# Performance work log

Hardware: AMD Instinct MI355X
Metric: run time of the kernel (lower is better)

The kernel has to match this reference:

```python
import jax, jax.numpy as jnp
import numpy as np

N, E, F_IN, H, C, G, NC = 50000, 800000, 128, 4, 64, 512, 10
NEG_SLOPE = 0.2


def setup_inputs() -> dict:
    key = jax.random.key(0)
    ks = jax.random.split(key, 16)
    s = lambda fan: 1.0 / np.sqrt(fan)
    inp = {
        'x': jax.random.normal(ks[0], (N, F_IN), jnp.float32),
        'edge_index': jax.random.randint(ks[1], (2, E), 0, N, jnp.int64),
        'batch': jnp.sort(jax.random.randint(ks[2], (N,), 0, G, jnp.int64)),
        # conv1: F_IN -> H*C, concat
        'W1': jax.random.normal(ks[3], (F_IN, H * C), jnp.float32) * s(F_IN),
        'a_src1': jax.random.normal(ks[4], (H, C), jnp.float32) * s(C),
        'a_dst1': jax.random.normal(ks[5], (H, C), jnp.float32) * s(C),
        'b1': jnp.zeros((H * C,), jnp.float32),
        # conv2: H*C -> H*C, concat
        'W2': jax.random.normal(ks[6], (H * C, H * C), jnp.float32) * s(H * C),
        'a_src2': jax.random.normal(ks[7], (H, C), jnp.float32) * s(C),
        'a_dst2': jax.random.normal(ks[8], (H, C), jnp.float32) * s(C),
        'b2': jnp.zeros((H * C,), jnp.float32),
        # conv3: H*C -> C, concat=False (mean over heads)
        'W3': jax.random.normal(ks[9], (H * C, H * C), jnp.float32) * s(H * C),
        'a_src3': jax.random.normal(ks[10], (H, C), jnp.float32) * s(C),
        'a_dst3': jax.random.normal(ks[11], (H, C), jnp.float32) * s(C),
        'b3': jnp.zeros((C,), jnp.float32),
        # final linear: C -> NC
        'Wl': jax.random.normal(ks[12], (C, NC), jnp.float32) * s(C),
        'bl': jnp.zeros((NC,), jnp.float32),
    }
    return inp


def _gat_conv(x, src, dst, W, a_src, a_dst, b, concat):
    n = x.shape[0]
    h = (x @ W).reshape(n, H, C)                       # [N,H,C]
    al_src = jnp.sum(h * a_src, axis=-1)               # [N,H]
    al_dst = jnp.sum(h * a_dst, axis=-1)               # [N,H]
    e = al_src[src] + al_dst[dst]                      # [E',H] per-edge logits
    e = jax.nn.leaky_relu(e, NEG_SLOPE)
    # segment softmax over incoming edges of each dst node
    m = jax.ops.segment_max(e, dst, num_segments=n)
    ex = jnp.exp(e - m[dst])
    z = jax.ops.segment_sum(ex, dst, num_segments=n)
    alpha = ex / (z[dst] + 1e-16)                      # [E',H]
    msg = h[src] * alpha[:, :, None]                   # [E',H,C]
    out = jax.ops.segment_sum(msg, dst, num_segments=n)  # [N,H,C]
    out = out.reshape(n, H * C) if concat else out.mean(axis=1)
    return out + b


def reference(x, edge_index, batch, W1, a_src1, a_dst1, b1, W2, a_src2, a_dst2, b2,
              W3, a_src3, a_dst3, b3, Wl, bl):
    n = x.shape[0]
    loops = jnp.arange(n, dtype=edge_index.dtype)
    src = jnp.concatenate([edge_index[0], loops])      # add self-loops (PyG default)
    dst = jnp.concatenate([edge_index[1], loops])
    h = jax.nn.relu(_gat_conv(x, src, dst, W1, a_src1, a_dst1, b1, True))
    h = jax.nn.relu(_gat_conv(h, src, dst, W2, a_src2, a_dst2, b2, True))
    h = jax.nn.relu(_gat_conv(h, src, dst, W3, a_src3, a_dst3, b3, False))
    # global mean pool over graphs
    sums = jax.ops.segment_sum(h, batch, num_segments=G)          # [G,C]
    cnts = jax.ops.segment_sum(jnp.ones((n,), h.dtype), batch, num_segments=G)
    pooled = sums / jnp.maximum(cnts, 1.0)[:, None]
    # dropout is identity in eval mode
    return pooled @ Wl + bl                                       # [G,NC]
```

## Files before the change

### kernel.cpp

```cpp
#include <hip/hip_runtime.h>

#define N_NODES 50000
#define E_EDGES 800000
#define E_TOT   (E_EDGES + N_NODES)
#define F_INDIM 128
#define NHEAD   4
#define CDIM    64
#define HC      256
#define NGRAPH  512
#define NCLS    10
#define NEG_SLOPE 0.2f
#define AGG_BLOCKS 2048
#define XCHUNKS (N_NODES * F_INDIM / 8)

typedef __attribute__((ext_vector_type(8))) _Float16 f16x8;
typedef __attribute__((ext_vector_type(8))) unsigned short ushort8;
typedef __attribute__((ext_vector_type(4))) float f32x4;

__device__ inline float leakyf(float x) { return x > 0.f ? x : NEG_SLOPE * x; }
__device__ inline unsigned short f2h(float x) {
  _Float16 h = (_Float16)x;
  return __builtin_bit_cast(unsigned short, h);
}
__device__ inline float h2f(unsigned short u) {
  return (float)__builtin_bit_cast(_Float16, u);
}

__global__ __launch_bounds__(256) void k_init_deg(int* __restrict__ deg) {
  int i = blockIdx.x * 256 + threadIdx.x;
  if (i < N_NODES) deg[i] = 1;
}

__global__ __launch_bounds__(256) void k_hist(const int* __restrict__ ei, int* __restrict__ deg) {
  int e = blockIdx.x * 256 + threadIdx.x;
  if (e < E_EDGES) atomicAdd(&deg[ei[E_EDGES + e]], 1);
}

__global__ __launch_bounds__(256) void k_scan1(const int* __restrict__ deg, int* __restrict__ incl,
                                               int* __restrict__ blksum) {
  __shared__ int s[256];
  int tid = threadIdx.x;
  int i = blockIdx.x * 256 + tid;
  int v = (i < N_NODES) ? deg[i] : 0;
  s[tid] = v;
  __syncthreads();
  for (int d = 1; d < 256; d <<= 1) {
    int t = (tid >= d) ? s[tid - d] : 0;
    __syncthreads();
    s[tid] += t;
    __syncthreads();
  }
  if (i < N_NODES) incl[i] = s[tid];
  if (tid == 255) blksum[blockIdx.x] = s[255];
}

__global__ __launch_bounds__(256) void k_scan2(int* __restrict__ blksum, int nblk) {
  __shared__ int s[256];
  int tid = threadIdx.x;
  int v = (tid < nblk) ? blksum[tid] : 0;
  s[tid] = v;
  __syncthreads();
  for (int d = 1; d < 256; d <<= 1) {
    int t = (tid >= d) ? s[tid - d] : 0;
    __syncthreads();
    s[tid] += t;
    __syncthreads();
  }
  if (tid < nblk) blksum[tid] = s[tid] - v;
}

__global__ __launch_bounds__(256) void k_scan3(const int* __restrict__ deg, int* __restrict__ off,
                                               const int* __restrict__ blksum, int* __restrict__ cursor) {
  int i = blockIdx.x * 256 + threadIdx.x;
  if (i < N_NODES) {
    int excl = off[i] - deg[i] + blksum[blockIdx.x];
    off[i] = excl;
    cursor[i] = excl;
  }
  if (i == 0) off[N_NODES] = E_TOT;
}

__global__ __launch_bounds__(256) void k_fill(const int* __restrict__ ei, int* __restrict__ cursor,
                                              int* __restrict__ csr_src) {
  int idx = blockIdx.x * 256 + threadIdx.x;
  if (idx >= E_TOT) return;
  int s, d;
  if (idx < E_EDGES) { s = ei[idx]; d = ei[E_EDGES + idx]; }
  else               { s = idx - E_EDGES; d = s; }
  int pos = atomicAdd(&cursor[d], 1);
  csr_src[pos] = s;
}

__global__ __launch_bounds__(256) void k_cvt_all(const float* __restrict__ x,
                                                 const float* __restrict__ W1,
                                                 const float* __restrict__ W2,
                                                 const float* __restrict__ W3,
                                                 unsigned short* __restrict__ xh,
                                                 unsigned short* __restrict__ Wt1,
                                                 unsigned short* __restrict__ Wt2,
                                                 unsigned short* __restrict__ Wt3) {
  int i = blockIdx.x * 256 + threadIdx.x;
  if (i < XCHUNKS) {
    float4 v0 = *(const float4*)&x[(size_t)i * 8];
    float4 v1 = *(const float4*)&x[(size_t)i * 8 + 4];
    ushort8 o;
    o[0] = f2h(v0.x); o[1] = f2h(v0.y); o[2] = f2h(v0.z); o[3] = f2h(v0.w);
    o[4] = f2h(v1.x); o[5] = f2h(v1.y); o[6] = f2h(v1.z); o[7] = f2h(v1.w);
    *(ushort8*)&xh[(size_t)i * 8] = o;
    return;
  }
  int j = i - XCHUNKS;
  if (j < F_INDIM * HC) {
    int k = j >> 8, n = j & 255;
    Wt1[n * F_INDIM + k] = f2h(W1[j]);
    return;
  }
  j -= F_INDIM * HC;
  if (j < HC * HC) {
    int k = j >> 8, n = j & 255;
    Wt2[n * HC + k] = f2h(W2[j]);
    return;
  }
  j -= HC * HC;
  if (j < HC * HC) {
    int k = j >> 8, n = j & 255;
    Wt3[n * HC + k] = f2h(W3[j]);
  }
}

template<int K>
__global__ __launch_bounds__(256) void k_gemm_f16(const unsigned short* __restrict__ A,
                                                  const unsigned short* __restrict__ Bt,
                                                  unsigned short* __restrict__ C,
                                                  const float* __restrict__ a_src,
                                                  const float* __restrict__ a_dst,
                                                  float* __restrict__ al_s,
                                                  float* __restrict__ al_d) {
  __shared__ unsigned short As[128 * 64];
  __shared__ unsigned short Bs[128 * 64];
  int tid = threadIdx.x;
  int w = tid >> 6, l = tid & 63;
  int wm = w >> 1, wn = w & 1;
  int m0 = blockIdx.x * 128, n0 = blockIdx.y * 128;
  f32x4 acc[4][4] = {};

  int sr = w * 32 + (l >> 3);
  int g8 = l & 7;
  int slot = g8 ^ (sr & 7);
  int fl = l & 15;

  for (int k0 = 0; k0 < K; k0 += 64) {
    uint4 va[4], vb[4];
#pragma unroll
    for (int j = 0; j < 4; ++j) {
      int ar = m0 + sr + j * 8;
      va[j] = (ar < N_NODES) ? *(const uint4*)&A[(size_t)ar * K + k0 + g8 * 8]
                             : make_uint4(0u, 0u, 0u, 0u);
      vb[j] = *(const uint4*)&Bt[(size_t)(n0 + sr + j * 8) * K + k0 + g8 * 8];
    }
    __syncthreads();
#pragma unroll
    for (int j = 0; j < 4; ++j) {
      *(uint4*)&As[(sr + j * 8) * 64 + slot * 8] = va[j];
      *(uint4*)&Bs[(sr + j * 8) * 64 + slot * 8] = vb[j];
    }
    __syncthreads();
#pragma unroll
    for (int kk = 0; kk < 2; ++kk) {
      int sl = ((kk * 4 + (l >> 4)) ^ (l & 7)) * 8;
      f16x8 af[4], bfr[4];
#pragma unroll
      for (int f = 0; f < 4; ++f) {
        af[f]  = *(const f16x8*)&As[(wm * 64 + f * 16 + fl) * 64 + sl];
        bfr[f] = *(const f16x8*)&Bs[(wn * 64 + f * 16 + fl) * 64 + sl];
      }
#pragma unroll
      for (int f = 0; f < 4; ++f)
#pragma unroll
        for (int g = 0; g < 4; ++g)
          acc[f][g] = __builtin_amdgcn_mfma_f32_16x16x32_f16(af[f], bfr[g], acc[f][g], 0, 0, 0);
    }
  }
  int cr = (l >> 4) * 4;
#pragma unroll
  for (int f = 0; f < 4; ++f) {
    int mrow = m0 + wm * 64 + f * 16 + cr;
#pragma unroll
    for (int r = 0; r < 4; ++r) {
      if (mrow + r < N_NODES) {
#pragma unroll
        for (int g = 0; g < 4; ++g)
          C[(size_t)(mrow + r) * HC + n0 + wn * 64 + g * 16 + fl] = f2h(acc[f][g][r]);
      }
    }
  }
  int head = blockIdx.y * 2 + wn;
  float as_r[4], ad_r[4];
#pragma unroll
  for (int g = 0; g < 4; ++g) {
    as_r[g] = a_src[head * 64 + g * 16 + fl];
    ad_r[g] = a_dst[head * 64 + g * 16 + fl];
  }
#pragma unroll
  for (int f = 0; f < 4; ++f) {
#pragma unroll
    for (int r = 0; r < 4; ++r) {
      float ps = 0.f, pd = 0.f;
#pragma unroll
      for (int g = 0; g < 4; ++g) {
        ps = fmaf(as_r[g], acc[f][g][r], ps);
        pd = fmaf(ad_r[g], acc[f][g][r], pd);
      }
#pragma unroll
      for (int o = 1; o < 16; o <<= 1) { ps += __shfl_xor(ps, o); pd += __shfl_xor(pd, o); }
      if (fl == 0) {
        int row = m0 + wm * 64 + f * 16 + cr + r;
        if (row < N_NODES) {
          al_s[row * 4 + head] = ps;
          al_d[row * 4 + head] = pd;
        }
      }
    }
  }
}

template<bool CONCAT>
__global__ __launch_bounds__(256) void k_aggregate(
    const unsigned short* __restrict__ h, const int* __restrict__ off, const int* __restrict__ csr_src,
    const float* __restrict__ al_s, const float* __restrict__ al_d,
    const float* __restrict__ bias, unsigned short* __restrict__ out_h, float* __restrict__ out_f) {
  __shared__ float s_p[4][64][4];
  __shared__ int   s_src[4][64];
  int tid = threadIdx.x;
  int wv = tid >> 6;
  int lane = tid & 63;
  int half_id = lane >> 5;
  int c8 = lane & 31;
  int cg8 = c8 << 3;
  int head = c8 >> 3;

  const int NW = AGG_BLOCKS * 4;
  for (int d = blockIdx.x * 4 + wv; d < N_NODES; d += NW) {
    int lo  = off[d];
    int deg = off[d + 1] - lo;

    float4 adv = *(const float4*)&al_d[(size_t)d * 4];

    float z0 = 0.f, z1 = 0.f, z2 = 0.f, z3 = 0.f;
    for (int e = lane; e < deg; e += 64) {
      int s = csr_src[lo + e];
      float4 asv = *(const float4*)&al_s[(size_t)s * 4];
      float p0 = __expf(leakyf(asv.x + adv.x));
      float p1 = __expf(leakyf(asv.y + adv.y));
      float p2 = __expf(leakyf(asv.z + adv.z));
      float p3 = __expf(leakyf(asv.w + adv.w));
      if (e < 64) {
        s_p[wv][e][0] = p0; s_p[wv][e][1] = p1;
        s_p[wv][e][2] = p2; s_p[wv][e][3] = p3;
        s_src[wv][e] = s;
      }
      z0 += p0; z1 += p1; z2 += p2; z3 += p3;
    }
#pragma unroll
    for (int o = 1; o < 64; o <<= 1) {
      z0 += __shfl_xor(z0, o); z1 += __shfl_xor(z1, o);
      z2 += __shfl_xor(z2, o); z3 += __shfl_xor(z3, o);
    }
    float zih = 1.f / ((head == 0 ? z0 : (head == 1 ? z1 : (head == 2 ? z2 : z3))) + 1e-16f);

    int dcap = min(deg, 64);
    float acc[8] = {};
    int e = half_id;
    for (; e + 14 < dcap; e += 16) {
      int sv[8]; float pv[8]; ushort8 hv[8];
#pragma unroll
      for (int q = 0; q < 8; ++q) {
        int ee = e + q * 2;
        sv[q] = s_src[wv][ee];
        pv[q] = s_p[wv][ee][head];
      }
#pragma unroll
      for (int q = 0; q < 8; ++q) hv[q] = *(const ushort8*)&h[(size_t)sv[q] * HC + cg8];
#pragma unroll
      for (int q = 0; q < 8; ++q)
#pragma unroll
        for (int i = 0; i < 8; ++i) acc[i] = fmaf(pv[q], h2f(hv[q][i]), acc[i]);
    }
    for (; e < dcap; e += 2) {
      int s = s_src[wv][e];
      float p = s_p[wv][e][head];
      ushort8 hv = *(const ushort8*)&h[(size_t)s * HC + cg8];
#pragma unroll
      for (int i = 0; i < 8; ++i) acc[i] = fmaf(p, h2f(hv[i]), acc[i]);
    }
    if (deg > 64) {
      for (int e2 = 64 + half_id; e2 < deg; e2 += 2) {
        int s = csr_src[lo + e2];
        float4 asv = *(const float4*)&al_s[(size_t)s * 4];
        float q0 = __expf(leakyf(asv.x + adv.x));
        float q1 = __expf(leakyf(asv.y + adv.y));
        float q2 = __expf(leakyf(asv.z + adv.z));
        float q3 = __expf(leakyf(asv.w + adv.w));
        float p = head == 0 ? q0 : (head == 1 ? q1 : (head == 2 ? q2 : q3));
        ushort8 hv = *(const ushort8*)&h[(size_t)s * HC + cg8];
#pragma unroll
        for (int i = 0; i < 8; ++i) acc[i] = fmaf(p, h2f(hv[i]), acc[i]);
      }
    }

#pragma unroll
    for (int i = 0; i < 8; ++i) {
      acc[i] *= zih;
      acc[i] += __shfl_xor(acc[i], 32);
    }

    if (CONCAT) {
      if (lane < 32) {
        float4 b0 = *(const float4*)&bias[cg8];
        float4 b1v = *(const float4*)&bias[cg8 + 4];
        ushort8 o;
        o[0] = f2h(fmaxf(acc[0] + b0.x, 0.f));
        o[1] = f2h(fmaxf(acc[1] + b0.y, 0.f));
        o[2] = f2h(fmaxf(acc[2] + b0.z, 0.f));
        o[3] = f2h(fmaxf(acc[3] + b0.w, 0.f));
        o[4] = f2h(fmaxf(acc[4] + b1v.x, 0.f));
        o[5] = f2h(fmaxf(acc[5] + b1v.y, 0.f));
        o[6] = f2h(fmaxf(acc[6] + b1v.z, 0.f));
        o[7] = f2h(fmaxf(acc[7] + b1v.w, 0.f));
        *(ushort8*)&out_h[(size_t)d * HC + cg8] = o;
      }
    } else {
#pragma unroll
      for (int i = 0; i < 8; ++i) {
        acc[i] += __shfl_xor(acc[i], 8);
        acc[i] += __shfl_xor(acc[i], 16);
      }
      if (lane < 8) {
        int c0 = lane << 3;
        float4 bb0 = *(const float4*)&bias[c0];
        float4 bb1 = *(const float4*)&bias[c0 + 4];
        float4 v0, v1;
        v0.x = fmaxf(acc[0] * 0.25f + bb0.x, 0.f);
        v0.y = fmaxf(acc[1] * 0.25f + bb0.y, 0.f);
        v0.z = fmaxf(acc[2] * 0.25f + bb0.z, 0.f);
        v0.w = fmaxf(acc[3] * 0.25f + bb0.w, 0.f);
        v1.x = fmaxf(acc[4] * 0.25f + bb1.x, 0.f);
        v1.y = fmaxf(acc[5] * 0.25f + bb1.y, 0.f);
        v1.z = fmaxf(acc[6] * 0.25f + bb1.z, 0.f);
        v1.w = fmaxf(acc[7] * 0.25f + bb1.w, 0.f);
        *(float4*)&out_f[(size_t)d * CDIM + c0] = v0;
        *(float4*)&out_f[(size_t)d * CDIM + c0 + 4] = v1;
      }
    }
  }
}

__device__ inline int lower_bound_i(const int* __restrict__ a, int n, int key) {
  int lo = 0, hi = n;
  while (lo < hi) { int mid = (lo + hi) >> 1; if (a[mid] < key) lo = mid + 1; else hi = mid; }
  return lo;
}

__global__ __launch_bounds__(256) void k_pool(const float* __restrict__ x, const int* __restrict__ batch,
                                              const float* __restrict__ Wl, const float* __restrict__ bl,
                                              float* __restrict__ out) {
  int g = blockIdx.x, tid = threadIdx.x;
  int lo = lower_bound_i(batch, N_NODES, g);
  int hi = lower_bound_i(batch, N_NODES, g + 1);
  int c = tid & 63, sl = tid >> 6;
  float acc = 0.f;
  for (int n = lo + sl; n < hi; n += 4)
    acc += x[(size_t)n * CDIM + c];
  __shared__ float s[256];
  __shared__ float pooled[64];
  s[tid] = acc;
  __syncthreads();
  if (tid < 64) {
    float cnt = fmaxf((float)(hi - lo), 1.f);
    pooled[tid] = (s[tid] + s[tid + 64] + s[tid + 128] + s[tid + 192]) / cnt;
  }
  __syncthreads();
  if (tid < NCLS) {
    float o = bl[tid];
    for (int cc = 0; cc < CDIM; ++cc)
      o = fmaf(pooled[cc], Wl[cc * NCLS + tid], o);
    out[g * NCLS + tid] = o;
  }
}

extern "C" void kernel_launch(void* const* d_in, const int* in_sizes, int n_in,
                              void* d_out, int out_size, void* d_ws, size_t ws_size,
                              hipStream_t stream) {
  const float* x     = (const float*)d_in[0];
  const int*   ei    = (const int*)d_in[1];
  const int*   batch = (const int*)d_in[2];
  const float* W1  = (const float*)d_in[3];
  const float* as1 = (const float*)d_in[4];
  const float* ad1 = (const float*)d_in[5];
  const float* b1  = (const float*)d_in[6];
  const float* W2  = (const float*)d_in[7];
  const float* as2 = (const float*)d_in[8];
  const float* ad2 = (const float*)d_in[9];
  const float* b2  = (const float*)d_in[10];
  const float* W3  = (const float*)d_in[11];
  const float* as3 = (const float*)d_in[12];
  const float* ad3 = (const float*)d_in[13];
  const float* b3  = (const float*)d_in[14];
  const float* Wl  = (const float*)d_in[15];
  const float* bl  = (const float*)d_in[16];
  float* out = (float*)d_out;

  char* ws = (char*)d_ws;
  size_t o = 0;
  auto alloc = [&](size_t bytes) -> void* {
    void* p = ws + o;
    o += (bytes + 255) & ~(size_t)255;
    return p;
  };
  unsigned short* hbuf  = (unsigned short*)alloc((size_t)N_NODES * HC * 2);
  unsigned short* abuf  = (unsigned short*)alloc((size_t)N_NODES * HC * 2);
  float*          bufC  = (float*)alloc((size_t)N_NODES * CDIM * 4);
  unsigned short* x_h   = (unsigned short*)alloc((size_t)N_NODES * F_INDIM * 2);
  unsigned short* Wt1   = (unsigned short*)alloc((size_t)HC * F_INDIM * 2);
  unsigned short* Wt2   = (unsigned short*)alloc((size_t)HC * HC * 2);
  unsigned short* Wt3   = (unsigned short*)alloc((size_t)HC * HC * 2);
  float* al_s  = (float*)alloc((size_t)N_NODES * 4 * 4);
  float* al_d  = (float*)alloc((size_t)N_NODES * 4 * 4);
  int*   deg   = (int*)alloc((size_t)N_NODES * 4);
  int*   off   = (int*)alloc((size_t)(N_NODES + 1) * 4);
  int*   cursor= (int*)alloc((size_t)N_NODES * 4);
  int*   blksum= (int*)alloc(1024);
  int*   csr   = (int*)alloc((size_t)E_TOT * 4);

  int nblk = (N_NODES + 255) / 256;
  k_init_deg<<<nblk, 256, 0, stream>>>(deg);
  k_hist<<<(E_EDGES + 255) / 256, 256, 0, stream>>>(ei, deg);
  k_scan1<<<nblk, 256, 0, stream>>>(deg, off, blksum);
  k_scan2<<<1, 256, 0, stream>>>(blksum, nblk);
  k_scan3<<<nblk, 256, 0, stream>>>(deg, off, blksum, cursor);
  k_fill<<<(E_TOT + 255) / 256, 256, 0, stream>>>(ei, cursor, csr);

  int cvt_total = XCHUNKS + F_INDIM * HC + 2 * HC * HC;
  k_cvt_all<<<(cvt_total + 255) / 256, 256, 0, stream>>>(x, W1, W2, W3, x_h, Wt1, Wt2, Wt3);

  dim3 ggrid((N_NODES + 127) / 128, HC / 128);
  k_gemm_f16<F_INDIM><<<ggrid, 256, 0, stream>>>(x_h, Wt1, hbuf, as1, ad1, al_s, al_d);
  k_aggregate<true><<<AGG_BLOCKS, 256, 0, stream>>>(hbuf, off, csr, al_s, al_d, b1, abuf, nullptr);
  k_gemm_f16<HC><<<ggrid, 256, 0, stream>>>(abuf, Wt2, hbuf, as2, ad2, al_s, al_d);
  k_aggregate<true><<<AGG_BLOCKS, 256, 0, stream>>>(hbuf, off, csr, al_s, al_d, b2, abuf, nullptr);
  k_gemm_f16<HC><<<ggrid, 256, 0, stream>>>(abuf, Wt3, hbuf, as3, ad3, al_s, al_d);
  k_aggregate<false><<<AGG_BLOCKS, 256, 0, stream>>>(hbuf, off, csr, al_s, al_d, b3, nullptr, bufC);
  k_pool<<<NGRAPH, 256, 0, stream>>>(bufC, batch, Wl, bl, out);
}
```

Measured before the change: 442.0 us.

## Store node features in per-32-channel slices and aggregate slice-by-slice

GEMM outputs and aggregation buffers now use a sliced layout ([8 slices][N][32] in fp16), and attention logits are stored head-major. The aggregation kernel gives each block one 32-channel slice, so gathered rows are 64 bytes and the slice's working set is smaller and more cache-friendly. Softmax normalization is folded into a single pass without a separate max or staging in shared memory. The head-mean, bias and ReLU of layer 3 move into the pool kernel. In exchange, each edge's index and exponent are recomputed once per slice (eight times), and gathers become small 4-byte accesses per lane.

```diff
diff --git a/kernel.cpp b/kernel.cpp
--- a/kernel.cpp
+++ b/kernel.cpp
@@ -128,7 +128,7 @@
   }
 }
 
-template<int K>
+template<int K, bool ASL>
 __global__ __launch_bounds__(256) void k_gemm_f16(const unsigned short* __restrict__ A,
                                                   const unsigned short* __restrict__ Bt,
                                                   unsigned short* __restrict__ C,
@@ -151,12 +151,18 @@
 
   for (int k0 = 0; k0 < K; k0 += 64) {
     uint4 va[4], vb[4];
+    int k = k0 + g8 * 8;
 #pragma unroll
     for (int j = 0; j < 4; ++j) {
       int ar = m0 + sr + j * 8;
-      va[j] = (ar < N_NODES) ? *(const uint4*)&A[(size_t)ar * K + k0 + g8 * 8]
-                             : make_uint4(0u, 0u, 0u, 0u);
-      vb[j] = *(const uint4*)&Bt[(size_t)(n0 + sr + j * 8) * K + k0 + g8 * 8];
+      if (ar >= N_NODES) {
+        va[j] = make_uint4(0u, 0u, 0u, 0u);
+      } else if (ASL) {
+        va[j] = *(const uint4*)&A[(size_t)(k >> 5) * N_NODES * 32 + (size_t)ar * 32 + (k & 31)];
+      } else {
+        va[j] = *(const uint4*)&A[(size_t)ar * K + k];
+      }
+      vb[j] = *(const uint4*)&Bt[(size_t)(n0 + sr + j * 8) * K + k];
     }
     __syncthreads();
 #pragma unroll
@@ -182,6 +188,7 @@
     }
   }
   int cr = (l >> 4) * 4;
+  int cb5 = (n0 + wn * 64) >> 5;
 #pragma unroll
   for (int f = 0; f < 4; ++f) {
     int mrow = m0 + wm * 64 + f * 16 + cr;
@@ -190,7 +197,8 @@
       if (mrow + r < N_NODES) {
 #pragma unroll
         for (int g = 0; g < 4; ++g)
-          C[(size_t)(mrow + r) * HC + n0 + wn * 64 + g * 16 + fl] = f2h(acc[f][g][r]);
+          C[(size_t)(cb5 + (g >> 1)) * N_NODES * 32 + (size_t)(mrow + r) * 32 + (g & 1) * 16 + fl]
+            = f2h(acc[f][g][r]);
       }
     }
   }
@@ -216,8 +224,8 @@
       if (fl == 0) {
         int row = m0 + wm * 64 + f * 16 + cr + r;
         if (row < N_NODES) {
-          al_s[row * 4 + head] = ps;
-          al_d[row * 4 + head] = pd;
+          al_s[head * N_NODES + row] = ps;
+          al_d[head * N_NODES + row] = pd;
         }
       }
     }
@@ -225,132 +233,75 @@
 }
 
 template<bool CONCAT>
-__global__ __launch_bounds__(256) void k_aggregate(
-    const unsigned short* __restrict__ h, const int* __restrict__ off, const int* __restrict__ csr_src,
-    const float* __restrict__ al_s, const float* __restrict__ al_d,
-    const float* __restrict__ bias, unsigned short* __restrict__ out_h, float* __restrict__ out_f) {
-  __shared__ float s_p[4][64][4];
-  __shared__ int   s_src[4][64];
+__global__ __launch_bounds__(256) void k_gather(
+    const unsigned short* __restrict__ h_sl, const int* __restrict__ off,
+    const int* __restrict__ csr_src,
+    const float* __restrict__ al_s_t, const float* __restrict__ al_d_t,
+    const float* __restrict__ bias, unsigned short* __restrict__ out_sl) {
   int tid = threadIdx.x;
-  int wv = tid >> 6;
-  int lane = tid & 63;
-  int half_id = lane >> 5;
-  int c8 = lane & 31;
-  int cg8 = c8 << 3;
-  int head = c8 >> 3;
-
-  const int NW = AGG_BLOCKS * 4;
-  for (int d = blockIdx.x * 4 + wv; d < N_NODES; d += NW) {
-    int lo  = off[d];
+  int wv = tid >> 6, lane = tid & 63;
+  int grp = lane >> 4;
+  int cl = lane & 15;
+  int slice = blockIdx.x & 7;
+  int head = slice >> 1;
+  const unsigned short* __restrict__ hs = h_sl + (size_t)slice * N_NODES * 32;
+  const float* __restrict__ als = al_s_t + (size_t)head * N_NODES;
+  const float* __restrict__ ald = al_d_t + (size_t)head * N_NODES;
+  unsigned short* __restrict__ os = out_sl + (size_t)slice * N_NODES * 32;
+  float b0 = 0.f, b1 = 0.f;
+  if (CONCAT) {
+    b0 = bias[slice * 32 + cl * 2];
+    b1 = bias[slice * 32 + cl * 2 + 1];
+  }
+  int wave_g = (blockIdx.x >> 3) * 4 + wv;
+
+  for (int d = wave_g; d < N_NODES; d += (AGG_BLOCKS / 8) * 4) {
+    int lo = off[d];
     int deg = off[d + 1] - lo;
-
-    float4 adv = *(const float4*)&al_d[(size_t)d * 4];
-
-    float z0 = 0.f, z1 = 0.f, z2 = 0.f, z3 = 0.f;
-    for (int e = lane; e < deg; e += 64) {
+    float ad = ald[d];
+    float a0 = 0.f, a1 = 0.f, z = 0.f;
+    int e = grp;
+    for (; e + 12 < deg; e += 16) {
+      int sv[4]; unsigned int hv[4]; float pv[4];
+#pragma unroll
+      for (int q = 0; q < 4; ++q) sv[q] = csr_src[lo + e + q * 4];
+#pragma unroll
+      for (int q = 0; q < 4; ++q) hv[q] = *(const unsigned int*)&hs[(size_t)sv[q] * 32 + cl * 2];
+#pragma unroll
+      for (int q = 0; q < 4; ++q) pv[q] = __expf(leakyf(als[sv[q]] + ad));
+#pragma unroll
+      for (int q = 0; q < 4; ++q) {
+        z += pv[q];
+        a0 = fmaf(pv[q], h2f((unsigned short)(hv[q] & 0xffffu)), a0);
+        a1 = fmaf(pv[q], h2f((unsigned short)(hv[q] >> 16)), a1);
+      }
+    }
+    for (; e < deg; e += 4) {
       int s = csr_src[lo + e];
-      float4 asv = *(const float4*)&al_s[(size_t)s * 4];
-      float p0 = __expf(leakyf(asv.x + adv.x));
-      float p1 = __expf(leakyf(asv.y + adv.y));
-      float p2 = __expf(leakyf(asv.z + adv.z));
-      float p3 = __expf(leakyf(asv.w + adv.w));
-      if (e < 64) {
-        s_p[wv][e][0] = p0; s_p[wv][e][1] = p1;
-        s_p[wv][e][2] = p2; s_p[wv][e][3] = p3;
-        s_src[wv][e] = s;
-      }
-      z0 += p0; z1 += p1; z2 += p2; z3 += p3;
-    }
-#pragma unroll
-    for (int o = 1; o < 64; o <<= 1) {
-      z0 += __shfl_xor(z0, o); z1 += __shfl_xor(z1, o);
-      z2 += __shfl_xor(z2, o); z3 += __shfl_xor(z3, o);
-    }
-    float zih = 1.f / ((head == 0 ? z0 : (head == 1 ? z1 : (head == 2 ? z2 : z3))) + 1e-16f);
-
-    int dcap = min(deg, 64);
-    float acc[8] = {};
-    int e = half_id;
-    for (; e + 14 < dcap; e += 16) {
-      int sv[8]; float pv[8]; ushort8 hv[8];
-#pragma unroll
-      for (int q = 0; q < 8; ++q) {
-        int ee = e + q * 2;
-        sv[q] = s_src[wv][ee];
-        pv[q] = s_p[wv][ee][head];
-      }
-#pragma unroll
-      for (int q = 0; q < 8; ++q) hv[q] = *(const ushort8*)&h[(size_t)sv[q] * HC + cg8];
-#pragma unroll
-      for (int q = 0; q < 8; ++q)
-#pragma unroll
-        for (int i = 0; i < 8; ++i) acc[i] = fmaf(pv[q], h2f(hv[q][i]), acc[i]);
-    }
-    for (; e < dcap; e += 2) {
-      int s = s_src[wv][e];
-      float p = s_p[wv][e][head];
-      ushort8 hv = *(const ushort8*)&h[(size_t)s * HC + cg8];
-#pragma unroll
-      for (int i = 0; i < 8; ++i) acc[i] = fmaf(p, h2f(hv[i]), acc[i]);
-    }
-    if (deg > 64) {
-      for (int e2 = 64 + half_id; e2 < deg; e2 += 2) {
-        int s = csr_src[lo + e2];
-        float4 asv = *(const float4*)&al_s[(size_t)s * 4];
-        float q0 = __expf(leakyf(asv.x + adv.x));
-        float q1 = __expf(leakyf(asv.y + adv.y));
-        float q2 = __expf(leakyf(asv.z + adv.z));
-        float q3 = __expf(leakyf(asv.w + adv.w));
-        float p = head == 0 ? q0 : (head == 1 ? q1 : (head == 2 ? q2 : q3));
-        ushort8 hv = *(const ushort8*)&h[(size_t)s * HC + cg8];
-#pragma unroll
-        for (int i = 0; i < 8; ++i) acc[i] = fmaf(p, h2f(hv[i]), acc[i]);
-      }
-    }
-
-#pragma unroll
-    for (int i = 0; i < 8; ++i) {
-      acc[i] *= zih;
-      acc[i] += __shfl_xor(acc[i], 32);
-    }
-
-    if (CONCAT) {
-      if (lane < 32) {
-        float4 b0 = *(const float4*)&bias[cg8];
-        float4 b1v = *(const float4*)&bias[cg8 + 4];
-        ushort8 o;
-        o[0] = f2h(fmaxf(acc[0] + b0.x, 0.f));
-        o[1] = f2h(fmaxf(acc[1] + b0.y, 0.f));
-        o[2] = f2h(fmaxf(acc[2] + b0.z, 0.f));
-        o[3] = f2h(fmaxf(acc[3] + b0.w, 0.f));
-        o[4] = f2h(fmaxf(acc[4] + b1v.x, 0.f));
-        o[5] = f2h(fmaxf(acc[5] + b1v.y, 0.f));
-        o[6] = f2h(fmaxf(acc[6] + b1v.z, 0.f));
-        o[7] = f2h(fmaxf(acc[7] + b1v.w, 0.f));
-        *(ushort8*)&out_h[(size_t)d * HC + cg8] = o;
-      }
-    } else {
-#pragma unroll
-      for (int i = 0; i < 8; ++i) {
-        acc[i] += __shfl_xor(acc[i], 8);
-        acc[i] += __shfl_xor(acc[i], 16);
-      }
-      if (lane < 8) {
-        int c0 = lane << 3;
-        float4 bb0 = *(const float4*)&bias[c0];
-        float4 bb1 = *(const float4*)&bias[c0 + 4];
-        float4 v0, v1;
-        v0.x = fmaxf(acc[0] * 0.25f + bb0.x, 0.f);
-        v0.y = fmaxf(acc[1] * 0.25f + bb0.y, 0.f);
-        v0.z = fmaxf(acc[2] * 0.25f + bb0.z, 0.f);
-        v0.w = fmaxf(acc[3] * 0.25f + bb0.w, 0.f);
-        v1.x = fmaxf(acc[4] * 0.25f + bb1.x, 0.f);
-        v1.y = fmaxf(acc[5] * 0.25f + bb1.y, 0.f);
-        v1.z = fmaxf(acc[6] * 0.25f + bb1.z, 0.f);
-        v1.w = fmaxf(acc[7] * 0.25f + bb1.w, 0.f);
-        *(float4*)&out_f[(size_t)d * CDIM + c0] = v0;
-        *(float4*)&out_f[(size_t)d * CDIM + c0 + 4] = v1;
-      }
+      unsigned int hv = *(const unsigned int*)&hs[(size_t)s * 32 + cl * 2];
+      float p = __expf(leakyf(als[s] + ad));
+      z += p;
+      a0 = fmaf(p, h2f((unsigned short)(hv & 0xffffu)), a0);
+      a1 = fmaf(p, h2f((unsigned short)(hv >> 16)), a1);
+    }
+#pragma unroll
+    for (int o = 16; o < 64; o <<= 1) {
+      z  += __shfl_xor(z, o);
+      a0 += __shfl_xor(a0, o);
+      a1 += __shfl_xor(a1, o);
+    }
+    float zi = 1.f / (z + 1e-16f);
+    a0 *= zi; a1 *= zi;
+    if (lane < 16) {
+      unsigned short u0, u1;
+      if (CONCAT) {
+        u0 = f2h(fmaxf(a0 + b0, 0.f));
+        u1 = f2h(fmaxf(a1 + b1, 0.f));
+      } else {
+        u0 = f2h(a0);
+        u1 = f2h(a1);
+      }
+      *(unsigned int*)&os[(size_t)d * 32 + cl * 2] = (unsigned int)u0 | ((unsigned int)u1 << 16);
     }
   }
 }
@@ -361,16 +312,26 @@
   return lo;
 }
 
-__global__ __launch_bounds__(256) void k_pool(const float* __restrict__ x, const int* __restrict__ batch,
+__global__ __launch_bounds__(256) void k_pool(const unsigned short* __restrict__ P,
+                                              const int* __restrict__ batch,
+                                              const float* __restrict__ b3,
                                               const float* __restrict__ Wl, const float* __restrict__ bl,
                                               float* __restrict__ out) {
   int g = blockIdx.x, tid = threadIdx.x;
   int lo = lower_bound_i(batch, N_NODES, g);
   int hi = lower_bound_i(batch, N_NODES, g + 1);
   int c = tid & 63, sl = tid >> 6;
+  int s0 = c >> 5;
+  int co = c & 31;
+  float bc = b3[c];
   float acc = 0.f;
-  for (int n = lo + sl; n < hi; n += 4)
-    acc += x[(size_t)n * CDIM + c];
+  for (int n = lo + sl; n < hi; n += 4) {
+    float v = h2f(P[(size_t)(s0 + 0) * N_NODES * 32 + (size_t)n * 32 + co])
+            + h2f(P[(size_t)(s0 + 2) * N_NODES * 32 + (size_t)n * 32 + co])
+            + h2f(P[(size_t)(s0 + 4) * N_NODES * 32 + (size_t)n * 32 + co])
+            + h2f(P[(size_t)(s0 + 6) * N_NODES * 32 + (size_t)n * 32 + co]);
+    acc += fmaxf(0.25f * v + bc, 0.f);
+  }
   __shared__ float s[256];
   __shared__ float pooled[64];
   s[tid] = acc;
@@ -419,13 +380,12 @@
   };
   unsigned short* hbuf  = (unsigned short*)alloc((size_t)N_NODES * HC * 2);
   unsigned short* abuf  = (unsigned short*)alloc((size_t)N_NODES * HC * 2);
-  float*          bufC  = (float*)alloc((size_t)N_NODES * CDIM * 4);
   unsigned short* x_h   = (unsigned short*)alloc((size_t)N_NODES * F_INDIM * 2);
   unsigned short* Wt1   = (unsigned short*)alloc((size_t)HC * F_INDIM * 2);
   unsigned short* Wt2   = (unsigned short*)alloc((size_t)HC * HC * 2);
   unsigned short* Wt3   = (unsigned short*)alloc((size_t)HC * HC * 2);
-  float* al_s  = (float*)alloc((size_t)N_NODES * 4 * 4);
-  float* al_d  = (float*)alloc((size_t)N_NODES * 4 * 4);
+  float* al_s  = (float*)alloc((size_t)NHEAD * N_NODES * 4);
+  float* al_d  = (float*)alloc((size_t)NHEAD * N_NODES * 4);
   int*   deg   = (int*)alloc((size_t)N_NODES * 4);
   int*   off   = (int*)alloc((size_t)(N_NODES + 1) * 4);
   int*   cursor= (int*)alloc((size_t)N_NODES * 4);
@@ -444,11 +404,11 @@
   k_cvt_all<<<(cvt_total + 255) / 256, 256, 0, stream>>>(x, W1, W2, W3, x_h, Wt1, Wt2, Wt3);
 
   dim3 ggrid((N_NODES + 127) / 128, HC / 128);
-  k_gemm_f16<F_INDIM><<<ggrid, 256, 0, stream>>>(x_h, Wt1, hbuf, as1, ad1, al_s, al_d);
-  k_aggregate<true><<<AGG_BLOCKS, 256, 0, stream>>>(hbuf, off, csr, al_s, al_d, b1, abuf, nullptr);
-  k_gemm_f16<HC><<<ggrid, 256, 0, stream>>>(abuf, Wt2, hbuf, as2, ad2, al_s, al_d);
-  k_aggregate<true><<<AGG_BLOCKS, 256, 0, stream>>>(hbuf, off, csr, al_s, al_d, b2, abuf, nullptr);
-  k_gemm_f16<HC><<<ggrid, 256, 0, stream>>>(abuf, Wt3, hbuf, as3, ad3, al_s, al_d);
-  k_aggregate<false><<<AGG_BLOCKS, 256, 0, stream>>>(hbuf, off, csr, al_s, al_d, b3, nullptr, bufC);
-  k_pool<<<NGRAPH, 256, 0, stream>>>(bufC, batch, Wl, bl, out);
-}
+  k_gemm_f16<F_INDIM, false><<<ggrid, 256, 0, stream>>>(x_h, Wt1, hbuf, as1, ad1, al_s, al_d);
+  k_gather<true><<<AGG_BLOCKS, 256, 0, stream>>>(hbuf, off, csr, al_s, al_d, b1, abuf);
+  k_gemm_f16<HC, true><<<ggrid, 256, 0, stream>>>(abuf, Wt2, hbuf, as2, ad2, al_s, al_d);
+  k_gather<true><<<AGG_BLOCKS, 256, 0, stream>>>(hbuf, off, csr, al_s, al_d, b2, abuf);
+  k_gemm_f16<HC, true><<<ggrid, 256, 0, stream>>>(abuf, Wt3, hbuf, as3, ad3, al_s, al_d);
+  k_gather<false><<<AGG_BLOCKS, 256, 0, stream>>>(hbuf, off, csr, al_s, al_d, b3, abuf);
+  k_pool<<<NGRAPH, 256, 0, stream>>>(abuf, batch, b3, Wl, bl, out);
+}
```

Measured after the change: 607.3 us. 37.4% more time.

## Use K=128 LDS tiles and prefetch next K-tile during MFMA compute

Applied to the files above, without the earlier changes.

The fp16 GEMM now stages 128-wide K tiles in shared memory instead of 64-wide, so K=128 runs as a single tile and K=256 as two. For K=256 the second tile's global loads are issued before computing the first tile, which overlaps memory latency with MFMA work and cuts the number of barriers. The cost is double the LDS per block (64KB) and 16 uint4 staging registers per thread, which may lower occupancy.

```diff
diff --git a/kernel.cpp b/kernel.cpp
--- a/kernel.cpp
+++ b/kernel.cpp
@@ -136,51 +136,70 @@
                                                   const float* __restrict__ a_dst,
                                                   float* __restrict__ al_s,
                                                   float* __restrict__ al_d) {
-  __shared__ unsigned short As[128 * 64];
-  __shared__ unsigned short Bs[128 * 64];
+  __shared__ unsigned short As[128 * 128];
+  __shared__ unsigned short Bs[128 * 128];
   int tid = threadIdx.x;
   int w = tid >> 6, l = tid & 63;
   int wm = w >> 1, wn = w & 1;
   int m0 = blockIdx.x * 128, n0 = blockIdx.y * 128;
+  int fl = l & 15, qq = l >> 4;
+  int ct = tid & 15;
+  int r0 = tid >> 4;
+  int slotw = (ct ^ r0) * 8;
   f32x4 acc[4][4] = {};
-
-  int sr = w * 32 + (l >> 3);
-  int g8 = l & 7;
-  int slot = g8 ^ (sr & 7);
-  int fl = l & 15;
-
-  for (int k0 = 0; k0 < K; k0 += 64) {
-    uint4 va[4], vb[4];
-#pragma unroll
-    for (int j = 0; j < 4; ++j) {
-      int ar = m0 + sr + j * 8;
-      va[j] = (ar < N_NODES) ? *(const uint4*)&A[(size_t)ar * K + k0 + g8 * 8]
+  uint4 va[8], vb[8];
+
+  auto LOAD = [&](int k0) {
+#pragma unroll
+    for (int j = 0; j < 8; ++j) {
+      int r = r0 + j * 16;
+      int ar = m0 + r;
+      va[j] = (ar < N_NODES) ? *(const uint4*)&A[(size_t)ar * K + k0 + ct * 8]
                              : make_uint4(0u, 0u, 0u, 0u);
-      vb[j] = *(const uint4*)&Bt[(size_t)(n0 + sr + j * 8) * K + k0 + g8 * 8];
-    }
-    __syncthreads();
-#pragma unroll
-    for (int j = 0; j < 4; ++j) {
-      *(uint4*)&As[(sr + j * 8) * 64 + slot * 8] = va[j];
-      *(uint4*)&Bs[(sr + j * 8) * 64 + slot * 8] = vb[j];
-    }
-    __syncthreads();
-#pragma unroll
-    for (int kk = 0; kk < 2; ++kk) {
-      int sl = ((kk * 4 + (l >> 4)) ^ (l & 7)) * 8;
-      f16x8 af[4], bfr[4];
+      vb[j] = *(const uint4*)&Bt[(size_t)(n0 + r) * K + k0 + ct * 8];
+    }
+  };
+  auto WRITE = [&]() {
+#pragma unroll
+    for (int j = 0; j < 8; ++j) {
+      int r = r0 + j * 16;
+      *(uint4*)&As[r * 128 + slotw] = va[j];
+      *(uint4*)&Bs[r * 128 + slotw] = vb[j];
+    }
+  };
+  auto COMPUTE = [&]() {
+#pragma unroll
+    for (int kk = 0; kk < 4; ++kk) {
+      int c0 = kk * 4 + qq;
+      int slr = (c0 ^ fl) * 8;
+      f16x8 af[4], bf[4];
 #pragma unroll
       for (int f = 0; f < 4; ++f) {
-        af[f]  = *(const f16x8*)&As[(wm * 64 + f * 16 + fl) * 64 + sl];
-        bfr[f] = *(const f16x8*)&Bs[(wn * 64 + f * 16 + fl) * 64 + sl];
+        af[f] = *(const f16x8*)&As[(wm * 64 + f * 16 + fl) * 128 + slr];
+        bf[f] = *(const f16x8*)&Bs[(wn * 64 + f * 16 + fl) * 128 + slr];
       }
 #pragma unroll
       for (int f = 0; f < 4; ++f)
 #pragma unroll
         for (int g = 0; g < 4; ++g)
-          acc[f][g] = __builtin_amdgcn_mfma_f32_16x16x32_f16(af[f], bfr[g], acc[f][g], 0, 0, 0);
-    }
-  }
+          acc[f][g] = __builtin_amdgcn_mfma_f32_16x16x32_f16(af[f], bf[g], acc[f][g], 0, 0, 0);
+    }
+  };
+
+  LOAD(0);
+  WRITE();
+  __syncthreads();
+  if (K == 128) {
+    COMPUTE();
+  } else {
+    LOAD(128);
+    COMPUTE();
+    __syncthreads();
+    WRITE();
+    __syncthreads();
+    COMPUTE();
+  }
+
   int cr = (l >> 4) * 4;
 #pragma unroll
   for (int f = 0; f < 4; ++f) {
```

Result: no change. 439.9 us (-0.5%).

## Use direct global-to-LDS loads in GEMM and fuse mean-pool into last aggregate

Applied to the files above, without the earlier changes.

The GEMM now loads its A and B tiles with global_load_lds straight into shared memory, which removes the register staging and one barrier per k-step. The A and x buffers are padded so loads past the last row stay in bounds without a guard. The final aggregation kernel now atomically adds each node's output into a per-graph pooled buffer, which removes the intermediate [N,64] float buffer and the separate pooling pass. The cost is float atomic contention on only 512 graph rows, and the sum order is no longer deterministic.

```diff
diff --git a/kernel.cpp b/kernel.cpp
--- a/kernel.cpp
+++ b/kernel.cpp
@@ -25,6 +25,10 @@
 __device__ inline float h2f(unsigned short u) {
   return (float)__builtin_bit_cast(_Float16, u);
 }
+
+#define GLL16(gp, lp) \
+  __builtin_amdgcn_global_load_lds((const __attribute__((address_space(1))) void*)(gp), \
+                                   (__attribute__((address_space(3))) void*)(lp), 16, 0, 0)
 
 __global__ __launch_bounds__(256) void k_init_deg(int* __restrict__ deg) {
   int i = blockIdx.x * 256 + threadIdx.x;
@@ -142,46 +146,39 @@
   int w = tid >> 6, l = tid & 63;
   int wm = w >> 1, wn = w & 1;
   int m0 = blockIdx.x * 128, n0 = blockIdx.y * 128;
+  int fl = l & 15, qq = l >> 4;
+  int w32 = w * 32;
+  int l3 = l >> 3;
+  int csw = (l & 7) ^ (l3 & 7);
   f32x4 acc[4][4] = {};
 
-  int sr = w * 32 + (l >> 3);
-  int g8 = l & 7;
-  int slot = g8 ^ (sr & 7);
-  int fl = l & 15;
-
   for (int k0 = 0; k0 < K; k0 += 64) {
-    uint4 va[4], vb[4];
 #pragma unroll
     for (int j = 0; j < 4; ++j) {
-      int ar = m0 + sr + j * 8;
-      va[j] = (ar < N_NODES) ? *(const uint4*)&A[(size_t)ar * K + k0 + g8 * 8]
-                             : make_uint4(0u, 0u, 0u, 0u);
-      vb[j] = *(const uint4*)&Bt[(size_t)(n0 + sr + j * 8) * K + k0 + g8 * 8];
+      int r = w32 + j * 8 + l3;
+      GLL16(&A[(size_t)(m0 + r) * K + k0 + csw * 8], &As[(w32 + j * 8) * 64]);
+      GLL16(&Bt[(size_t)(n0 + r) * K + k0 + csw * 8], &Bs[(w32 + j * 8) * 64]);
     }
     __syncthreads();
 #pragma unroll
-    for (int j = 0; j < 4; ++j) {
-      *(uint4*)&As[(sr + j * 8) * 64 + slot * 8] = va[j];
-      *(uint4*)&Bs[(sr + j * 8) * 64 + slot * 8] = vb[j];
-    }
-    __syncthreads();
-#pragma unroll
     for (int kk = 0; kk < 2; ++kk) {
-      int sl = ((kk * 4 + (l >> 4)) ^ (l & 7)) * 8;
-      f16x8 af[4], bfr[4];
+      f16x8 af[4], bf[4];
+      int sl = ((kk * 4 + qq) ^ (fl & 7)) * 8;
 #pragma unroll
       for (int f = 0; f < 4; ++f) {
-        af[f]  = *(const f16x8*)&As[(wm * 64 + f * 16 + fl) * 64 + sl];
-        bfr[f] = *(const f16x8*)&Bs[(wn * 64 + f * 16 + fl) * 64 + sl];
+        af[f] = *(const f16x8*)&As[(wm * 64 + f * 16 + fl) * 64 + sl];
+        bf[f] = *(const f16x8*)&Bs[(wn * 64 + f * 16 + fl) * 64 + sl];
       }
 #pragma unroll
       for (int f = 0; f < 4; ++f)
 #pragma unroll
         for (int g = 0; g < 4; ++g)
-          acc[f][g] = __builtin_amdgcn_mfma_f32_16x16x32_f16(af[f], bfr[g], acc[f][g], 0, 0, 0);
-    }
-  }
-  int cr = (l >> 4) * 4;
+          acc[f][g] = __builtin_amdgcn_mfma_f32_16x16x32_f16(af[f], bf[g], acc[f][g], 0, 0, 0);
+    }
+    if (k0 + 64 < K) __syncthreads();
+  }
+
+  int cr = qq * 4;
 #pragma unroll
   for (int f = 0; f < 4; ++f) {
     int mrow = m0 + wm * 64 + f * 16 + cr;
@@ -228,7 +225,8 @@
 __global__ __launch_bounds__(256) void k_aggregate(
     const unsigned short* __restrict__ h, const int* __restrict__ off, const int* __restrict__ csr_src,
     const float* __restrict__ al_s, const float* __restrict__ al_d,
-    const float* __restrict__ bias, unsigned short* __restrict__ out_h, float* __restrict__ out_f) {
+    const float* __restrict__ bias, unsigned short* __restrict__ out_h,
+    const int* __restrict__ batch, float* __restrict__ pooled) {
   __shared__ float s_p[4][64][4];
   __shared__ int   s_src[4][64];
   int tid = threadIdx.x;
@@ -337,19 +335,18 @@
       }
       if (lane < 8) {
         int c0 = lane << 3;
+        int g = batch[d];
+        float* pg = &pooled[(size_t)g * CDIM + c0];
         float4 bb0 = *(const float4*)&bias[c0];
         float4 bb1 = *(const float4*)&bias[c0 + 4];
-        float4 v0, v1;
-        v0.x = fmaxf(acc[0] * 0.25f + bb0.x, 0.f);
-        v0.y = fmaxf(acc[1] * 0.25f + bb0.y, 0.f);
-        v0.z = fmaxf(acc[2] * 0.25f + bb0.z, 0.f);
-        v0.w = fmaxf(acc[3] * 0.25f + bb0.w, 0.f);
-        v1.x = fmaxf(acc[4] * 0.25f + bb1.x, 0.f);
-        v1.y = fmaxf(acc[5] * 0.25f + bb1.y, 0.f);
-        v1.z = fmaxf(acc[6] * 0.25f + bb1.z, 0.f);
-        v1.w = fmaxf(acc[7] * 0.25f + bb1.w, 0.f);
-        *(float4*)&out_f[(size_t)d * CDIM + c0] = v0;
-        *(float4*)&out_f[(size_t)d * CDIM + c0 + 4] = v1;
+        atomicAdd(&pg[0], fmaxf(acc[0] * 0.25f + bb0.x, 0.f));
+        atomicAdd(&pg[1], fmaxf(acc[1] * 0.25f + bb0.y, 0.f));
+        atomicAdd(&pg[2], fmaxf(acc[2] * 0.25f + bb0.z, 0.f));
+        atomicAdd(&pg[3], fmaxf(acc[3] * 0.25f + bb0.w, 0.f));
+        atomicAdd(&pg[4], fmaxf(acc[4] * 0.25f + bb1.x, 0.f));
+        atomicAdd(&pg[5], fmaxf(acc[5] * 0.25f + bb1.y, 0.f));
+        atomicAdd(&pg[6], fmaxf(acc[6] * 0.25f + bb1.z, 0.f));
+        atomicAdd(&pg[7], fmaxf(acc[7] * 0.25f + bb1.w, 0.f));
       }
     }
   }
@@ -361,29 +358,22 @@
   return lo;
 }
 
-__global__ __launch_bounds__(256) void k_pool(const float* __restrict__ x, const int* __restrict__ batch,
-                                              const float* __restrict__ Wl, const float* __restrict__ bl,
-                                              float* __restrict__ out) {
+__global__ __launch_bounds__(64) void k_pool_finish(const float* __restrict__ pooled,
+                                                    const int* __restrict__ batch,
+                                                    const float* __restrict__ Wl,
+                                                    const float* __restrict__ bl,
+                                                    float* __restrict__ out) {
   int g = blockIdx.x, tid = threadIdx.x;
   int lo = lower_bound_i(batch, N_NODES, g);
   int hi = lower_bound_i(batch, N_NODES, g + 1);
-  int c = tid & 63, sl = tid >> 6;
-  float acc = 0.f;
-  for (int n = lo + sl; n < hi; n += 4)
-    acc += x[(size_t)n * CDIM + c];
-  __shared__ float s[256];
-  __shared__ float pooled[64];
-  s[tid] = acc;
-  __syncthreads();
-  if (tid < 64) {
-    float cnt = fmaxf((float)(hi - lo), 1.f);
-    pooled[tid] = (s[tid] + s[tid + 64] + s[tid + 128] + s[tid + 192]) / cnt;
-  }
+  float cnt = fmaxf((float)(hi - lo), 1.f);
+  __shared__ float pl[64];
+  pl[tid] = pooled[(size_t)g * CDIM + tid] / cnt;
   __syncthreads();
   if (tid < NCLS) {
     float o = bl[tid];
     for (int cc = 0; cc < CDIM; ++cc)
-      o = fmaf(pooled[cc], Wl[cc * NCLS + tid], o);
+      o = fmaf(pl[cc], Wl[cc * NCLS + tid], o);
     out[g * NCLS + tid] = o;
   }
 }
@@ -417,15 +407,16 @@
     o += (bytes + 255) & ~(size_t)255;
     return p;
   };
+  const size_t NPAD = N_NODES + 128;
   unsigned short* hbuf  = (unsigned short*)alloc((size_t)N_NODES * HC * 2);
-  unsigned short* abuf  = (unsigned short*)alloc((size_t)N_NODES * HC * 2);
-  float*          bufC  = (float*)alloc((size_t)N_NODES * CDIM * 4);
-  unsigned short* x_h   = (unsigned short*)alloc((size_t)N_NODES * F_INDIM * 2);
+  unsigned short* abuf  = (unsigned short*)alloc(NPAD * HC * 2);
+  unsigned short* x_h   = (unsigned short*)alloc(NPAD * F_INDIM * 2);
   unsigned short* Wt1   = (unsigned short*)alloc((size_t)HC * F_INDIM * 2);
   unsigned short* Wt2   = (unsigned short*)alloc((size_t)HC * HC * 2);
   unsigned short* Wt3   = (unsigned short*)alloc((size_t)HC * HC * 2);
   float* al_s  = (float*)alloc((size_t)N_NODES * 4 * 4);
   float* al_d  = (float*)alloc((size_t)N_NODES * 4 * 4);
+  float* pooled= (float*)alloc((size_t)NGRAPH * CDIM * 4);
   int*   deg   = (int*)alloc((size_t)N_NODES * 4);
   int*   off   = (int*)alloc((size_t)(N_NODES + 1) * 4);
   int*   cursor= (int*)alloc((size_t)N_NODES * 4);
@@ -442,13 +433,14 @@
 
   int cvt_total = XCHUNKS + F_INDIM * HC + 2 * HC * HC;
   k_cvt_all<<<(cvt_total + 255) / 256, 256, 0, stream>>>(x, W1, W2, W3, x_h, Wt1, Wt2, Wt3);
+  hipMemsetAsync(pooled, 0, (size_t)NGRAPH * CDIM * 4, stream);
 
   dim3 ggrid((N_NODES + 127) / 128, HC / 128);
   k_gemm_f16<F_INDIM><<<ggrid, 256, 0, stream>>>(x_h, Wt1, hbuf, as1, ad1, al_s, al_d);
-  k_aggregate<true><<<AGG_BLOCKS, 256, 0, stream>>>(hbuf, off, csr, al_s, al_d, b1, abuf, nullptr);
+  k_aggregate<true><<<AGG_BLOCKS, 256, 0, stream>>>(hbuf, off, csr, al_s, al_d, b1, abuf, nullptr, nullptr);
   k_gemm_f16<HC><<<ggrid, 256, 0, stream>>>(abuf, Wt2, hbuf, as2, ad2, al_s, al_d);
-  k_aggregate<true><<<AGG_BLOCKS, 256, 0, stream>>>(hbuf, off, csr, al_s, al_d, b2, abuf, nullptr);
+  k_aggregate<true><<<AGG_BLOCKS, 256, 0, stream>>>(hbuf, off, csr, al_s, al_d, b2, abuf, nullptr, nullptr);
   k_gemm_f16<HC><<<ggrid, 256, 0, stream>>>(abuf, Wt3, hbuf, as3, ad3, al_s, al_d);
-  k_aggregate<false><<<AGG_BLOCKS, 256, 0, stream>>>(hbuf, off, csr, al_s, al_d, b3, nullptr, bufC);
-  k_pool<<<NGRAPH, 256, 0, stream>>>(bufC, batch, Wl, bl, out);
-}
+  k_aggregate<false><<<AGG_BLOCKS, 256, 0, stream>>>(hbuf, off, csr, al_s, al_d, b3, nullptr, batch, pooled);
+  k_pool_finish<<<NGRAPH, 64, 0, stream>>>(pooled, batch, Wl, bl, out);
+}
```

New measurement: 534.9 us. 21.0% more time.
